# Kernel optimization log

Hardware: AMD Instinct MI355X
Metric: run time of the kernel (lower is better)

The kernel has to match this reference:

```python
import jax, jax.numpy as jnp
import numpy as np

N = 50000      # num_nodes
E = 800000     # num_edges (before self-loops)
IN_C = 128
HID = 64       # per-head channels (concat=False -> heads averaged)
HEADS = 4
OUT_C = 128
NEG_SLOPE = 0.2
EPS = 1e-5


def setup_inputs() -> dict:
    key = jax.random.key(0)
    ks = jax.random.split(key, 12)
    p = lambda k, shape: jax.random.normal(k, shape, dtype=jnp.float32) * 0.1
    inp = {
        "x": jax.random.normal(ks[0], (N, IN_C), dtype=jnp.float32),
        "edge_index": jax.random.randint(ks[1], (2, E), 0, N, dtype=jnp.int32),
        # layer 1 GATConv params
        "W1": p(ks[2], (IN_C, HEADS * HID)),
        "asrc1": p(ks[3], (HEADS, HID)),
        "adst1": p(ks[4], (HEADS, HID)),
        "b1": jnp.zeros((HID,), jnp.float32),
        "g1": jnp.ones((HID,), jnp.float32),
        "be1": jnp.zeros((HID,), jnp.float32),
        # layer 2 GATConv params
        "W2": p(ks[5], (HID, HEADS * HID)),
        "asrc2": p(ks[6], (HEADS, HID)),
        "adst2": p(ks[7], (HEADS, HID)),
        "b2": jnp.zeros((HID,), jnp.float32),
        "g2": jnp.ones((HID,), jnp.float32),
        "be2": jnp.zeros((HID,), jnp.float32),
        # output projection
        "Wo": p(ks[8], (HID, OUT_C)),
        "bo": jnp.zeros((OUT_C,), jnp.float32),
    }
    return inp


def _gat(x, W, asrc, adst, b, src, dst):
    """PyG GATConv (shared lin, concat=False -> mean over heads, + bias)."""
    n = x.shape[0]
    h = (x @ W).reshape(n, HEADS, HID)          # [N,H,C]
    es = jnp.sum(h * asrc, axis=-1)             # [N,H] alpha_src
    ed = jnp.sum(h * adst, axis=-1)             # [N,H] alpha_dst
    e = jax.nn.leaky_relu(es[src] + ed[dst], NEG_SLOPE)  # [E,H]
    # segment softmax over edges grouped by destination node
    emax = jax.ops.segment_max(e, dst, num_segments=n)
    ex = jnp.exp(e - emax[dst])
    den = jax.ops.segment_sum(ex, dst, num_segments=n)
    alpha = ex / den[dst]                       # [E,H]
    msg = h[src] * alpha[:, :, None]            # [E,H,C]
    out = jax.ops.segment_sum(msg, dst, num_segments=n)  # [N,H,C]
    return out.mean(axis=1) + b                 # concat=False -> head mean


def _ln(x, g, b):
    m = x.mean(-1, keepdims=True)
    v = x.var(-1, keepdims=True)
    return (x - m) / jnp.sqrt(v + EPS) * g + b


def reference(x, edge_index, W1, asrc1, adst1, b1, g1, be1,
              W2, asrc2, adst2, b2, g2, be2, Wo, bo):
    n = x.shape[0]
    loop = jnp.arange(n, dtype=edge_index.dtype)   # GATConv add_self_loops=True
    src = jnp.concatenate([edge_index[0], loop])
    dst = jnp.concatenate([edge_index[1], loop])
    h = jax.nn.relu(_ln(_gat(x, W1, asrc1, adst1, b1, src, dst), g1, be1))
    h = jax.nn.relu(_ln(_gat(h, W2, asrc2, adst2, b2, src, dst), g2, be2))
    return h @ Wo + bo
```

## Files before the change

### kernel.cpp

```cpp
#include <hip/hip_runtime.h>

#define NHEADS 4
#define NEG_SLOPE 0.2f
#define EPS_LN 1e-5f
#define BCAP 64
#define POOLCAP 1536
#define BIN_EPB 8192
#define MAX_NS 800

typedef __attribute__((ext_vector_type(8))) short bf16x8;
typedef __attribute__((ext_vector_type(4))) float f32x4;

__global__ __launch_bounds__(256) void k_init_deg(int* __restrict__ deg, int n) {
    int i = blockIdx.x * 256 + threadIdx.x;
    if (i < n) deg[i] = 1;
}

__global__ __launch_bounds__(256) void k_count(const int* __restrict__ dst, int* __restrict__ deg, int e) {
    int i = blockIdx.x * 256 + threadIdx.x;
    if (i < e) atomicAdd(&deg[dst[i]], 1);
}

__global__ __launch_bounds__(256) void k_scan1(const int* __restrict__ deg, int* __restrict__ rs,
                                               int* __restrict__ bsum, int n) {
    __shared__ int tmp[256];
    int tx = threadIdx.x;
    int i = blockIdx.x * 256 + tx;
    int v = (i < n) ? deg[i] : 0;
    tmp[tx] = v;
    __syncthreads();
    for (int off = 1; off < 256; off <<= 1) {
        int t = (tx >= off) ? tmp[tx - off] : 0;
        __syncthreads();
        tmp[tx] += t;
        __syncthreads();
    }
    if (i < n) rs[i] = tmp[tx] - v;
    if (tx == 255) bsum[blockIdx.x] = tmp[255];
}

__global__ __launch_bounds__(256) void k_scan2(int* __restrict__ bsum, int nb) {
    __shared__ int tmp[256];
    int tx = threadIdx.x;
    int v = (tx < nb) ? bsum[tx] : 0;
    tmp[tx] = v;
    __syncthreads();
    for (int off = 1; off < 256; off <<= 1) {
        int t = (tx >= off) ? tmp[tx - off] : 0;
        __syncthreads();
        tmp[tx] += t;
        __syncthreads();
    }
    if (tx < nb) bsum[tx] = tmp[tx] - v;
}

__global__ __launch_bounds__(256) void k_scan3(int* __restrict__ rs, int* __restrict__ cur,
                                               const int* __restrict__ bsum, int n, int total) {
    int i = blockIdx.x * 256 + threadIdx.x;
    if (i < n) {
        int r = rs[i] + bsum[blockIdx.x];
        rs[i] = r;
        cur[i] = r;
    }
    if (i == 0) rs[n] = total;
}

__global__ __launch_bounds__(256) void k_scatter(const int* __restrict__ src, const int* __restrict__ dst,
                                                 int* __restrict__ cur, int* __restrict__ col, int e, int n) {
    int i = blockIdx.x * 256 + threadIdx.x;
    if (i < e + n) {
        int s, d;
        if (i < e) { s = src[i]; d = dst[i]; }
        else       { s = i - e;  d = i - e;  }
        int p = atomicAdd(&cur[d], 1);
        col[p] = s;
    }
}

__device__ __forceinline__ unsigned short cvt_bf16(float x) {
    unsigned u = __float_as_uint(x);
    u += 0x7fffu + ((u >> 16) & 1u);
    return (unsigned short)(u >> 16);
}

__device__ __forceinline__ unsigned pack2_bf16(float a, float b) {
    return (unsigned)cvt_bf16(a) | ((unsigned)cvt_bf16(b) << 16);
}

__global__ __launch_bounds__(256) void k_bin(const int* __restrict__ e_src, const int* __restrict__ e_dst,
                                             int* __restrict__ cursor, unsigned* __restrict__ pool,
                                             int E, int NS) {
    __shared__ unsigned staged[BIN_EPB];
    __shared__ unsigned short st_sl[BIN_EPB];
    __shared__ int scnt[MAX_NS], sprefix[MAX_NS], scur[MAX_NS], gbase[MAX_NS];
    __shared__ int tsum[256];
    int t = threadIdx.x;
    int b0 = blockIdx.x * BIN_EPB;
    for (int s = t; s < NS; s += 256) { scnt[s] = 0; scur[s] = 0; }
    __syncthreads();
    for (int k = 0; k < BIN_EPB / 256; k++) {
        int i = b0 + k * 256 + t;
        if (i < E) atomicAdd(&scnt[e_dst[i] >> 6], 1);
    }
    __syncthreads();
    int per = (NS + 255) / 256;
    int s0 = t * per;
    int acc = 0;
    for (int k = 0; k < per; k++) { int idx = s0 + k; if (idx < NS) acc += scnt[idx]; }
    tsum[t] = acc;
    __syncthreads();
    for (int off = 1; off < 256; off <<= 1) {
        int v = (t >= off) ? tsum[t - off] : 0;
        __syncthreads();
        tsum[t] += v;
        __syncthreads();
    }
    int run = (t == 0) ? 0 : tsum[t - 1];
    for (int k = 0; k < per; k++) {
        int idx = s0 + k;
        if (idx < NS) { sprefix[idx] = run; run += scnt[idx]; }
    }
    for (int s = t; s < NS; s += 256)
        gbase[s] = atomicAdd(&cursor[s], scnt[s]);
    __syncthreads();
    for (int k = 0; k < BIN_EPB / 256; k++) {
        int i = b0 + k * 256 + t;
        if (i < E) {
            int d = e_dst[i];
            int s = e_src[i];
            int sl = d >> 6;
            int p = atomicAdd(&scur[sl], 1);
            int pos = sprefix[sl] + p;
            staged[pos] = (unsigned)s | ((unsigned)(d & 63) << 20);
            st_sl[pos] = (unsigned short)sl;
        }
    }
    __syncthreads();
    int ec = E - b0; if (ec > BIN_EPB) ec = BIN_EPB; if (ec < 0) ec = 0;
    for (int i = t; i < ec; i += 256) {
        unsigned e = staged[i];
        int sl = st_sl[i];
        int off = i - sprefix[sl];
        int gp = gbase[sl] + off;
        if (gp < POOLCAP) pool[(size_t)sl * POOLCAP + gp] = e;
    }
}

template <int K>
__global__ __launch_bounds__(256) void k_gemm_gat(const float* __restrict__ A, const float* __restrict__ B,
                                                  const float* __restrict__ asrc, const float* __restrict__ adst,
                                                  unsigned short* __restrict__ Hb16, float* __restrict__ es,
                                                  float* __restrict__ ed, int M) {
    __shared__ unsigned short Bt[128][136];
    int tid = threadIdx.x;
    int m0 = blockIdx.x * 128;
    int n0 = blockIdx.y * 128;
    {
        int n = tid & 127;
        int kh = tid >> 7;
        int kbeg = kh * (K >> 1);
        int kend = kbeg + (K >> 1);
        const float* bp = B + n0 + n;
#pragma unroll 4
        for (int k = kbeg; k < kend; k += 4) {
            float b0 = bp[(size_t)k * 256];
            float b1 = bp[(size_t)(k + 1) * 256];
            float b2 = bp[(size_t)(k + 2) * 256];
            float b3 = bp[(size_t)(k + 3) * 256];
            uint2 p;
            p.x = pack2_bf16(b0, b1);
            p.y = pack2_bf16(b2, b3);
            *(uint2*)&Bt[n][k] = p;
        }
    }
    __syncthreads();
    int w = tid >> 6, lane = tid & 63;
    int quad = lane >> 4, col16 = lane & 15;
    int mw = m0 + (w >> 1) * 64;
    int ch = w & 1;
    int head = blockIdx.y * 2 + ch;
    f32x4 acc[4][4] = {};
    constexpr int kc = K >> 5;
#pragma unroll 2
    for (int c = 0; c < kc; c++) {
        int kb = c * 32 + quad * 8;
        bf16x8 afr[4], bfr[4];
#pragma unroll
        for (int i = 0; i < 4; i++) {
            int row = mw + i * 16 + col16;
            if (row >= M) row = M - 1;
            const float* ap = &A[(size_t)row * K + kb];
            float4 a0 = *(const float4*)ap;
            float4 a1 = *(const float4*)(ap + 4);
            bf16x8 t;
            t[0] = (short)cvt_bf16(a0.x); t[1] = (short)cvt_bf16(a0.y);
            t[2] = (short)cvt_bf16(a0.z); t[3] = (short)cvt_bf16(a0.w);
            t[4] = (short)cvt_bf16(a1.x); t[5] = (short)cvt_bf16(a1.y);
            t[6] = (short)cvt_bf16(a1.z); t[7] = (short)cvt_bf16(a1.w);
            afr[i] = t;
        }
#pragma unroll
        for (int j = 0; j < 4; j++)
            bfr[j] = *(const bf16x8*)&Bt[ch * 64 + j * 16 + col16][kb];
#pragma unroll
        for (int i = 0; i < 4; i++)
#pragma unroll
            for (int j = 0; j < 4; j++)
                acc[i][j] = __builtin_amdgcn_mfma_f32_16x16x32_bf16(afr[i], bfr[j], acc[i][j], 0, 0, 0);
    }
    float av[4], dv[4];
#pragma unroll
    for (int j = 0; j < 4; j++) {
        av[j] = asrc[head * 64 + j * 16 + col16];
        dv[j] = adst[head * 64 + j * 16 + col16];
    }
#pragma unroll
    for (int i = 0; i < 4; i++) {
#pragma unroll
        for (int r = 0; r < 4; r++) {
            int m = mw + i * 16 + quad * 4 + r;
            float se = acc[i][0][r] * av[0] + acc[i][1][r] * av[1]
                     + acc[i][2][r] * av[2] + acc[i][3][r] * av[3];
            float sd = acc[i][0][r] * dv[0] + acc[i][1][r] * dv[1]
                     + acc[i][2][r] * dv[2] + acc[i][3][r] * dv[3];
            se += __shfl_xor(se, 1, 64); sd += __shfl_xor(sd, 1, 64);
            se += __shfl_xor(se, 2, 64); sd += __shfl_xor(sd, 2, 64);
            se += __shfl_xor(se, 4, 64); sd += __shfl_xor(sd, 4, 64);
            se += __shfl_xor(se, 8, 64); sd += __shfl_xor(sd, 8, 64);
            if (m < M) {
#pragma unroll
                for (int j = 0; j < 4; j++)
                    Hb16[(size_t)m * 256 + head * 64 + j * 16 + col16] = cvt_bf16(acc[i][j][r]);
                if (col16 == 0) { es[m * 4 + head] = se; ed[m * 4 + head] = sd; }
            }
        }
    }
}

__global__ __launch_bounds__(256) void k_gemm(const float* __restrict__ A, const float* __restrict__ B,
                                              const float* __restrict__ bias, float* __restrict__ C,
                                              int M, int Nn, int K) {
    __shared__ unsigned short Al[128][72];
    __shared__ unsigned short Bt[128][72];
    int tid = threadIdx.x;
    int m0 = blockIdx.x * 128;
    {
        int n = tid & 127;
        int kh = tid >> 7;
        int kbeg = kh * (K >> 1);
        int kend = kbeg + (K >> 1);
        const float* bp = B + n;
        for (int k = kbeg; k < kend; k += 4) {
            float b0 = bp[(size_t)k * Nn];
            float b1 = bp[(size_t)(k + 1) * Nn];
            float b2 = bp[(size_t)(k + 2) * Nn];
            float b3 = bp[(size_t)(k + 3) * Nn];
            uint2 p;
            p.x = pack2_bf16(b0, b1);
            p.y = pack2_bf16(b2, b3);
            *(uint2*)&Bt[n][k] = p;
        }
    }
#pragma unroll
    for (int it = 0; it < 8; it++) {
        int idx = it * 256 + tid;
        int row = idx >> 4;
        int kq = (idx & 15) << 2;
        float4 a4 = make_float4(0.f, 0.f, 0.f, 0.f);
        if (m0 + row < M) a4 = *(const float4*)&A[(size_t)(m0 + row) * 64 + kq];
        uint2 p;
        p.x = pack2_bf16(a4.x, a4.y);
        p.y = pack2_bf16(a4.z, a4.w);
        *(uint2*)&Al[row][kq] = p;
    }
    __syncthreads();
    int w = tid >> 6, lane = tid & 63;
    int quad = lane >> 4, col16 = lane & 15;
    int rw = (w >> 1) * 64;
    int ch = w & 1;
    f32x4 acc[4][4] = {};
    int kc = K >> 5;
    for (int c = 0; c < kc; c++) {
        int kb = c * 32 + quad * 8;
        bf16x8 afr[4], bfr[4];
#pragma unroll
        for (int i = 0; i < 4; i++)
            afr[i] = *(const bf16x8*)&Al[rw + i * 16 + col16][kb];
#pragma unroll
        for (int j = 0; j < 4; j++)
            bfr[j] = *(const bf16x8*)&Bt[ch * 64 + j * 16 + col16][kb];
#pragma unroll
        for (int i = 0; i < 4; i++)
#pragma unroll
            for (int j = 0; j < 4; j++)
                acc[i][j] = __builtin_amdgcn_mfma_f32_16x16x32_bf16(afr[i], bfr[j], acc[i][j], 0, 0, 0);
    }
    int mw = m0 + rw;
    float bv[4];
#pragma unroll
    for (int j = 0; j < 4; j++) bv[j] = bias[ch * 64 + j * 16 + col16];
#pragma unroll
    for (int i = 0; i < 4; i++) {
#pragma unroll
        for (int r = 0; r < 4; r++) {
            int m = mw + i * 16 + quad * 4 + r;
            if (m < M) {
#pragma unroll
                for (int j = 0; j < 4; j++)
                    C[(size_t)m * Nn + ch * 64 + j * 16 + col16] = acc[i][j][r] + bv[j];
            }
        }
    }
}

__global__ __launch_bounds__(512) void k_agg_sliced(const unsigned* __restrict__ Hb, const float* __restrict__ es,
                                                    const float* __restrict__ ed, const unsigned* __restrict__ pool,
                                                    const int* __restrict__ cursor, const float* __restrict__ b,
                                                    const float* __restrict__ g, const float* __restrict__ be,
                                                    float* __restrict__ out, int n) {
    __shared__ unsigned ent[POOLCAP];
    __shared__ int lcnt[64], lbase[65], lcur[64];
    int t = threadIdx.x;
    int sl = blockIdx.x;
    if (t < 64) { lcnt[t] = 0; lcur[t] = 0; }
    __syncthreads();
    int ne = cursor[sl]; if (ne > POOLCAP) ne = POOLCAP;
    for (int i = t; i < ne; i += 512)
        atomicAdd(&lcnt[pool[(size_t)sl * POOLCAP + i] >> 20], 1);
    __syncthreads();
    if (t == 0) {
        int run = 0;
        for (int k = 0; k < 64; k++) { lbase[k] = run; run += lcnt[k]; }
        lbase[64] = run;
    }
    __syncthreads();
    for (int i = t; i < ne; i += 512) {
        unsigned e = pool[(size_t)sl * POOLCAP + i];
        int ln = e >> 20;
        int p = atomicAdd(&lcur[ln], 1);
        ent[lbase[ln] + p] = e & 0xFFFFFu;
    }
    __syncthreads();
    int wv = t >> 6, lane = t & 63;
    int head = lane >> 4, cp = lane & 15;
    for (int j = 0; j < 8; j++) {
        int ln = wv * 8 + j;
        int node = sl * 64 + ln;
        if (node >= n) continue;
        float edv = ed[node * 4 + head];
        float eS = es[node * 4 + head] + edv;
        eS = fmaxf(eS, NEG_SLOPE * eS);
        float wS = __expf(eS);
        uint2 uS = *(const uint2*)&Hb[(size_t)node * 128 + lane * 2];
        float acc0 = wS * __uint_as_float(uS.x << 16);
        float acc1 = wS * __uint_as_float(uS.x & 0xffff0000u);
        float acc2 = wS * __uint_as_float(uS.y << 16);
        float acc3 = wS * __uint_as_float(uS.y & 0xffff0000u);
        float den = wS;
        int i0 = lbase[ln], i1 = lbase[ln] + lcnt[ln];
        int i = i0;
        for (; i + 3 < i1; i += 4) {
            int s0 = ent[i], s1 = ent[i + 1], s2 = ent[i + 2], s3 = ent[i + 3];
            float e0 = es[s0 * 4 + head];
            float e1 = es[s1 * 4 + head];
            float e2 = es[s2 * 4 + head];
            float e3 = es[s3 * 4 + head];
            uint2 u0 = *(const uint2*)&Hb[(size_t)s0 * 128 + lane * 2];
            uint2 u1 = *(const uint2*)&Hb[(size_t)s1 * 128 + lane * 2];
            uint2 u2 = *(const uint2*)&Hb[(size_t)s2 * 128 + lane * 2];
            uint2 u3 = *(const uint2*)&Hb[(size_t)s3 * 128 + lane * 2];
            e0 += edv; e1 += edv; e2 += edv; e3 += edv;
            e0 = fmaxf(e0, NEG_SLOPE * e0);
            e1 = fmaxf(e1, NEG_SLOPE * e1);
            e2 = fmaxf(e2, NEG_SLOPE * e2);
            e3 = fmaxf(e3, NEG_SLOPE * e3);
            float w0 = __expf(e0), w1 = __expf(e1), w2 = __expf(e2), w3 = __expf(e3);
            acc0 += w0 * __uint_as_float(u0.x << 16);
            acc1 += w0 * __uint_as_float(u0.x & 0xffff0000u);
            acc2 += w0 * __uint_as_float(u0.y << 16);
            acc3 += w0 * __uint_as_float(u0.y & 0xffff0000u);
            acc0 += w1 * __uint_as_float(u1.x << 16);
            acc1 += w1 * __uint_as_float(u1.x & 0xffff0000u);
            acc2 += w1 * __uint_as_float(u1.y << 16);
            acc3 += w1 * __uint_as_float(u1.y & 0xffff0000u);
            acc0 += w2 * __uint_as_float(u2.x << 16);
            acc1 += w2 * __uint_as_float(u2.x & 0xffff0000u);
            acc2 += w2 * __uint_as_float(u2.y << 16);
            acc3 += w2 * __uint_as_float(u2.y & 0xffff0000u);
            acc0 += w3 * __uint_as_float(u3.x << 16);
            acc1 += w3 * __uint_as_float(u3.x & 0xffff0000u);
            acc2 += w3 * __uint_as_float(u3.y << 16);
            acc3 += w3 * __uint_as_float(u3.y & 0xffff0000u);
            den += w0 + w1 + w2 + w3;
        }
        for (; i < i1; i++) {
            int s0 = ent[i];
            float e0 = es[s0 * 4 + head] + edv;
            uint2 u0 = *(const uint2*)&Hb[(size_t)s0 * 128 + lane * 2];
            e0 = fmaxf(e0, NEG_SLOPE * e0);
            float w0 = __expf(e0);
            acc0 += w0 * __uint_as_float(u0.x << 16);
            acc1 += w0 * __uint_as_float(u0.x & 0xffff0000u);
            acc2 += w0 * __uint_as_float(u0.y << 16);
            acc3 += w0 * __uint_as_float(u0.y & 0xffff0000u);
            den += w0;
        }
        float rd = 1.f / den;
        float r0 = acc0 * rd, r1 = acc1 * rd, r2 = acc2 * rd, r3 = acc3 * rd;
        r0 += __shfl_xor(r0, 16, 64); r1 += __shfl_xor(r1, 16, 64);
        r2 += __shfl_xor(r2, 16, 64); r3 += __shfl_xor(r3, 16, 64);
        r0 += __shfl_xor(r0, 32, 64); r1 += __shfl_xor(r1, 32, 64);
        r2 += __shfl_xor(r2, 32, 64); r3 += __shfl_xor(r3, 32, 64);
        float4 bb = *(const float4*)&b[cp * 4];
        float v0 = 0.25f * r0 + bb.x;
        float v1 = 0.25f * r1 + bb.y;
        float v2 = 0.25f * r2 + bb.z;
        float v3 = 0.25f * r3 + bb.w;
        float s = v0 + v1 + v2 + v3;
        float q = v0 * v0 + v1 * v1 + v2 * v2 + v3 * v3;
        for (int off = 1; off < 16; off <<= 1) {
            s += __shfl_xor(s, off, 64);
            q += __shfl_xor(q, off, 64);
        }
        float mean = s * (1.f / 64.f);
        float var = q * (1.f / 64.f) - mean * mean;
        float rinv = rsqrtf(var + EPS_LN);
        float4 gg = *(const float4*)&g[cp * 4];
        float4 ee = *(const float4*)&be[cp * 4];
        if (head == 0) {
            float4 y;
            y.x = fmaxf((v0 - mean) * rinv * gg.x + ee.x, 0.f);
            y.y = fmaxf((v1 - mean) * rinv * gg.y + ee.y, 0.f);
            y.z = fmaxf((v2 - mean) * rinv * gg.z + ee.z, 0.f);
            y.w = fmaxf((v3 - mean) * rinv * gg.w + ee.w, 0.f);
            *(float4*)&out[(size_t)node * 64 + cp * 4] = y;
        }
    }
}

__global__ __launch_bounds__(256) void k_gat_aggregate(const unsigned* __restrict__ Hb, const float* __restrict__ es,
                                                       const float* __restrict__ ed, const int* __restrict__ rs,
                                                       const int* __restrict__ col,
                                                       const float* __restrict__ b,
                                                       const float* __restrict__ g, const float* __restrict__ be,
                                                       float* __restrict__ out, int n) {
    int node = blockIdx.x * 4 + (threadIdx.x >> 6);
    int lane = threadIdx.x & 63;
    if (node >= n) return;
    int head = lane >> 4;
    int cp = lane & 15;
    float edv = ed[node * 4 + head];
    float acc0 = 0.f, acc1 = 0.f, acc2 = 0.f, acc3 = 0.f, den = 0.f;
    int i0 = rs[node], i1 = rs[node + 1];
    int i = i0;
    for (; i + 3 < i1; i += 4) {
        int s0 = col[i], s1 = col[i + 1], s2 = col[i + 2], s3 = col[i + 3];
        float e0 = es[s0 * 4 + head];
        float e1 = es[s1 * 4 + head];
        float e2 = es[s2 * 4 + head];
        float e3 = es[s3 * 4 + head];
        uint2 u0 = *(const uint2*)&Hb[(size_t)s0 * 128 + lane * 2];
        uint2 u1 = *(const uint2*)&Hb[(size_t)s1 * 128 + lane * 2];
        uint2 u2 = *(const uint2*)&Hb[(size_t)s2 * 128 + lane * 2];
        uint2 u3 = *(const uint2*)&Hb[(size_t)s3 * 128 + lane * 2];
        e0 += edv; e1 += edv; e2 += edv; e3 += edv;
        e0 = fmaxf(e0, NEG_SLOPE * e0);
        e1 = fmaxf(e1, NEG_SLOPE * e1);
        e2 = fmaxf(e2, NEG_SLOPE * e2);
        e3 = fmaxf(e3, NEG_SLOPE * e3);
        float w0 = __expf(e0), w1 = __expf(e1), w2 = __expf(e2), w3 = __expf(e3);
        acc0 += w0 * __uint_as_float(u0.x << 16);
        acc1 += w0 * __uint_as_float(u0.x & 0xffff0000u);
        acc2 += w0 * __uint_as_float(u0.y << 16);
        acc3 += w0 * __uint_as_float(u0.y & 0xffff0000u);
        acc0 += w1 * __uint_as_float(u1.x << 16);
        acc1 += w1 * __uint_as_float(u1.x & 0xffff0000u);
        acc2 += w1 * __uint_as_float(u1.y << 16);
        acc3 += w1 * __uint_as_float(u1.y & 0xffff0000u);
        acc0 += w2 * __uint_as_float(u2.x << 16);
        acc1 += w2 * __uint_as_float(u2.x & 0xffff0000u);
        acc2 += w2 * __uint_as_float(u2.y << 16);
        acc3 += w2 * __uint_as_float(u2.y & 0xffff0000u);
        acc0 += w3 * __uint_as_float(u3.x << 16);
        acc1 += w3 * __uint_as_float(u3.x & 0xffff0000u);
        acc2 += w3 * __uint_as_float(u3.y << 16);
        acc3 += w3 * __uint_as_float(u3.y & 0xffff0000u);
        den += w0 + w1 + w2 + w3;
    }
    for (; i < i1; i++) {
        int s0 = col[i];
        float e0 = es[s0 * 4 + head] + edv;
        uint2 u0 = *(const uint2*)&Hb[(size_t)s0 * 128 + lane * 2];
        e0 = fmaxf(e0, NEG_SLOPE * e0);
        float w0 = __expf(e0);
        acc0 += w0 * __uint_as_float(u0.x << 16);
        acc1 += w0 * __uint_as_float(u0.x & 0xffff0000u);
        acc2 += w0 * __uint_as_float(u0.y << 16);
        acc3 += w0 * __uint_as_float(u0.y & 0xffff0000u);
        den += w0;
    }
    float rd = 1.f / den;
    float r0 = acc0 * rd, r1 = acc1 * rd, r2 = acc2 * rd, r3 = acc3 * rd;
    r0 += __shfl_xor(r0, 16, 64); r1 += __shfl_xor(r1, 16, 64);
    r2 += __shfl_xor(r2, 16, 64); r3 += __shfl_xor(r3, 16, 64);
    r0 += __shfl_xor(r0, 32, 64); r1 += __shfl_xor(r1, 32, 64);
    r2 += __shfl_xor(r2, 32, 64); r3 += __shfl_xor(r3, 32, 64);
    float4 bb = *(const float4*)&b[cp * 4];
    float v0 = 0.25f * r0 + bb.x;
    float v1 = 0.25f * r1 + bb.y;
    float v2 = 0.25f * r2 + bb.z;
    float v3 = 0.25f * r3 + bb.w;
    float s = v0 + v1 + v2 + v3;
    float q = v0 * v0 + v1 * v1 + v2 * v2 + v3 * v3;
    for (int off = 1; off < 16; off <<= 1) {
        s += __shfl_xor(s, off, 64);
        q += __shfl_xor(q, off, 64);
    }
    float mean = s * (1.f / 64.f);
    float var = q * (1.f / 64.f) - mean * mean;
    float rinv = rsqrtf(var + EPS_LN);
    float4 gg = *(const float4*)&g[cp * 4];
    float4 ee = *(const float4*)&be[cp * 4];
    if (head == 0) {
        float4 y;
        y.x = fmaxf((v0 - mean) * rinv * gg.x + ee.x, 0.f);
        y.y = fmaxf((v1 - mean) * rinv * gg.y + ee.y, 0.f);
        y.z = fmaxf((v2 - mean) * rinv * gg.z + ee.z, 0.f);
        y.w = fmaxf((v3 - mean) * rinv * gg.w + ee.w, 0.f);
        *(float4*)&out[(size_t)node * 64 + cp * 4] = y;
    }
}

extern "C" void kernel_launch(void* const* d_in, const int* in_sizes, int n_in,
                              void* d_out, int out_size, void* d_ws, size_t ws_size,
                              hipStream_t stream) {
    const float* x     = (const float*)d_in[0];
    const int*   eidx  = (const int*)d_in[1];
    const float* W1    = (const float*)d_in[2];
    const float* asrc1 = (const float*)d_in[3];
    const float* adst1 = (const float*)d_in[4];
    const float* b1    = (const float*)d_in[5];
    const float* g1    = (const float*)d_in[6];
    const float* be1   = (const float*)d_in[7];
    const float* W2    = (const float*)d_in[8];
    const float* asrc2 = (const float*)d_in[9];
    const float* adst2 = (const float*)d_in[10];
    const float* b2    = (const float*)d_in[11];
    const float* g2    = (const float*)d_in[12];
    const float* be2   = (const float*)d_in[13];
    const float* Wo    = (const float*)d_in[14];
    const float* bo    = (const float*)d_in[15];

    const int N = in_sizes[0] / 128;
    const int E = in_sizes[1] / 2;
    const int* srcp = eidx;
    const int* dstp = eidx + E;

    unsigned* hb   = (unsigned*)d_ws;
    float* h_small = (float*)(hb + (size_t)N * 128);
    float* es      = h_small + (size_t)N * 64;
    float* ed      = es + (size_t)N * 4;
    int* tail      = (int*)(ed + (size_t)N * 4);

    const int nb = (N + 255) / 256;
    const int nwb = (N + 3) / 4;
    const int mt128 = (N + 127) / 128;
    const int NS = (N + 63) >> 6;

    size_t prefix_bytes = (size_t)((char*)tail - (char*)d_ws);
    size_t pool_need = prefix_bytes + (size_t)NS * POOLCAP * 4 + (size_t)NS * 4;

    unsigned* pool = (unsigned*)tail;
    int* cursor = (int*)(pool + (size_t)NS * POOLCAP);

    int* rowstart = nullptr; int* colarr = nullptr;
    bool pooled = (ws_size >= pool_need) && (NS <= MAX_NS);

    if (pooled) {
        hipMemsetAsync(cursor, 0, (size_t)NS * 4, stream);
        k_bin<<<(E + BIN_EPB - 1) / BIN_EPB, 256, 0, stream>>>(srcp, dstp, cursor, pool, E, NS);
    } else {
        int* deg  = tail;
        rowstart  = deg + N;
        int* cur  = rowstart + (N + 1);
        colarr    = cur + N;
        int* bsum = colarr + (size_t)(E + N);
        k_init_deg<<<nb, 256, 0, stream>>>(deg, N);
        k_count<<<(E + 255) / 256, 256, 0, stream>>>(dstp, deg, E);
        k_scan1<<<nb, 256, 0, stream>>>(deg, rowstart, bsum, N);
        k_scan2<<<1, 256, 0, stream>>>(bsum, nb);
        k_scan3<<<nb, 256, 0, stream>>>(rowstart, cur, bsum, N, E + N);
        k_scatter<<<(E + N + 255) / 256, 256, 0, stream>>>(srcp, dstp, cur, colarr, E, N);
    }

    k_gemm_gat<128><<<dim3(mt128, 2), 256, 0, stream>>>(x, W1, asrc1, adst1,
                                                        (unsigned short*)hb, es, ed, N);
    if (pooled)
        k_agg_sliced<<<NS, 512, 0, stream>>>(hb, es, ed, pool, cursor, b1, g1, be1, h_small, N);
    else
        k_gat_aggregate<<<nwb, 256, 0, stream>>>(hb, es, ed, rowstart, colarr, b1, g1, be1, h_small, N);

    k_gemm_gat<64><<<dim3(mt128, 2), 256, 0, stream>>>(h_small, W2, asrc2, adst2,
                                                       (unsigned short*)hb, es, ed, N);
    if (pooled)
        k_agg_sliced<<<NS, 512, 0, stream>>>(hb, es, ed, pool, cursor, b2, g2, be2, h_small, N);
    else
        k_gat_aggregate<<<nwb, 256, 0, stream>>>(hb, es, ed, rowstart, colarr, b2, g2, be2, h_small, N);

    k_gemm<<<mt128, 256, 0, stream>>>(h_small, Wo, bo, (float*)d_out, N, 128, 64);
}
```

Before: 347.1 us.

## Stage A tile in LDS for GEMM and split aggregation across half-wave edge slots

The GEMM now converts each A tile to bf16 once into shared memory, so the four waves no longer each reload and reconvert overlapping rows from global memory. In the sliced aggregation kernel, each wave handles two edges at a time: each half-wave covers one edge and each lane loads 8 bf16 channels with a uint4, then a cross-half shuffle combines the partial sums before the head-mean and layernorm. The serial prefix over local counts is replaced by a wave shuffle scan. The trade-offs are extra shared memory and barriers in the GEMM, and predicated dummy loads on odd edge counts in aggregation.

```diff
diff --git a/kernel.cpp b/kernel.cpp
--- a/kernel.cpp
+++ b/kernel.cpp
@@ -3,7 +3,6 @@
 #define NHEADS 4
 #define NEG_SLOPE 0.2f
 #define EPS_LN 1e-5f
-#define BCAP 64
 #define POOLCAP 1536
 #define BIN_EPB 8192
 #define MAX_NS 800
@@ -86,6 +85,9 @@
 __device__ __forceinline__ unsigned pack2_bf16(float a, float b) {
     return (unsigned)cvt_bf16(a) | ((unsigned)cvt_bf16(b) << 16);
 }
+
+__device__ __forceinline__ float blo(unsigned u) { return __uint_as_float(u << 16); }
+__device__ __forceinline__ float bhi(unsigned u) { return __uint_as_float(u & 0xffff0000u); }
 
 __global__ __launch_bounds__(256) void k_bin(const int* __restrict__ e_src, const int* __restrict__ e_dst,
                                              int* __restrict__ cursor, unsigned* __restrict__ pool,
@@ -152,6 +154,7 @@
                                                   unsigned short* __restrict__ Hb16, float* __restrict__ es,
                                                   float* __restrict__ ed, int M) {
     __shared__ unsigned short Bt[128][136];
+    __shared__ unsigned short Al[128][72];
     int tid = threadIdx.x;
     int m0 = blockIdx.x * 128;
     int n0 = blockIdx.y * 128;
@@ -173,41 +176,48 @@
             *(uint2*)&Bt[n][k] = p;
         }
     }
-    __syncthreads();
     int w = tid >> 6, lane = tid & 63;
     int quad = lane >> 4, col16 = lane & 15;
-    int mw = m0 + (w >> 1) * 64;
+    int rw = (w >> 1) * 64;
     int ch = w & 1;
     int head = blockIdx.y * 2 + ch;
     f32x4 acc[4][4] = {};
-    constexpr int kc = K >> 5;
-#pragma unroll 2
-    for (int c = 0; c < kc; c++) {
-        int kb = c * 32 + quad * 8;
-        bf16x8 afr[4], bfr[4];
-#pragma unroll
-        for (int i = 0; i < 4; i++) {
-            int row = mw + i * 16 + col16;
-            if (row >= M) row = M - 1;
-            const float* ap = &A[(size_t)row * K + kb];
-            float4 a0 = *(const float4*)ap;
-            float4 a1 = *(const float4*)(ap + 4);
-            bf16x8 t;
-            t[0] = (short)cvt_bf16(a0.x); t[1] = (short)cvt_bf16(a0.y);
-            t[2] = (short)cvt_bf16(a0.z); t[3] = (short)cvt_bf16(a0.w);
-            t[4] = (short)cvt_bf16(a1.x); t[5] = (short)cvt_bf16(a1.y);
-            t[6] = (short)cvt_bf16(a1.z); t[7] = (short)cvt_bf16(a1.w);
-            afr[i] = t;
-        }
-#pragma unroll
-        for (int j = 0; j < 4; j++)
-            bfr[j] = *(const bf16x8*)&Bt[ch * 64 + j * 16 + col16][kb];
-#pragma unroll
-        for (int i = 0; i < 4; i++)
+    constexpr int KH = (K > 64) ? 2 : 1;
+    for (int h = 0; h < KH; h++) {
+        __syncthreads();
+#pragma unroll
+        for (int it = 0; it < 8; it++) {
+            int idx = it * 256 + tid;
+            int row = idx >> 4;
+            int kq = (idx & 15) << 2;
+            float4 a4 = make_float4(0.f, 0.f, 0.f, 0.f);
+            int gr = m0 + row;
+            if (gr < M) a4 = *(const float4*)&A[(size_t)gr * K + h * 64 + kq];
+            uint2 p;
+            p.x = pack2_bf16(a4.x, a4.y);
+            p.y = pack2_bf16(a4.z, a4.w);
+            *(uint2*)&Al[row][kq] = p;
+        }
+        __syncthreads();
+#pragma unroll
+        for (int c = 0; c < 2; c++) {
+            int kbl = c * 32 + quad * 8;
+            int kb = h * 64 + kbl;
+            bf16x8 afr[4], bfr[4];
+#pragma unroll
+            for (int i = 0; i < 4; i++)
+                afr[i] = *(const bf16x8*)&Al[rw + i * 16 + col16][kbl];
 #pragma unroll
             for (int j = 0; j < 4; j++)
-                acc[i][j] = __builtin_amdgcn_mfma_f32_16x16x32_bf16(afr[i], bfr[j], acc[i][j], 0, 0, 0);
-    }
+                bfr[j] = *(const bf16x8*)&Bt[ch * 64 + j * 16 + col16][kb];
+#pragma unroll
+            for (int i = 0; i < 4; i++)
+#pragma unroll
+                for (int j = 0; j < 4; j++)
+                    acc[i][j] = __builtin_amdgcn_mfma_f32_16x16x32_bf16(afr[i], bfr[j], acc[i][j], 0, 0, 0);
+        }
+    }
+    int mw = m0 + rw;
     float av[4], dv[4];
 #pragma unroll
     for (int j = 0; j < 4; j++) {
@@ -328,10 +338,15 @@
     for (int i = t; i < ne; i += 512)
         atomicAdd(&lcnt[pool[(size_t)sl * POOLCAP + i] >> 20], 1);
     __syncthreads();
-    if (t == 0) {
-        int run = 0;
-        for (int k = 0; k < 64; k++) { lbase[k] = run; run += lcnt[k]; }
-        lbase[64] = run;
+    if (t < 64) {
+        int v = lcnt[t];
+        int x = v;
+        for (int off = 1; off < 64; off <<= 1) {
+            int y = __shfl_up(x, off, 64);
+            if (t >= off) x += y;
+        }
+        lbase[t] = x - v;
+        if (t == 63) lbase[64] = x;
     }
     __syncthreads();
     for (int i = t; i < ne; i += 512) {
@@ -342,98 +357,96 @@
     }
     __syncthreads();
     int wv = t >> 6, lane = t & 63;
-    int head = lane >> 4, cp = lane & 15;
+    int slot = lane >> 5;
+    int sub = lane & 31;
+    int headL = sub >> 3;
+    int grp = sub & 7;
     for (int j = 0; j < 8; j++) {
         int ln = wv * 8 + j;
         int node = sl * 64 + ln;
         if (node >= n) continue;
-        float edv = ed[node * 4 + head];
-        float eS = es[node * 4 + head] + edv;
-        eS = fmaxf(eS, NEG_SLOPE * eS);
-        float wS = __expf(eS);
-        uint2 uS = *(const uint2*)&Hb[(size_t)node * 128 + lane * 2];
-        float acc0 = wS * __uint_as_float(uS.x << 16);
-        float acc1 = wS * __uint_as_float(uS.x & 0xffff0000u);
-        float acc2 = wS * __uint_as_float(uS.y << 16);
-        float acc3 = wS * __uint_as_float(uS.y & 0xffff0000u);
-        float den = wS;
-        int i0 = lbase[ln], i1 = lbase[ln] + lcnt[ln];
-        int i = i0;
-        for (; i + 3 < i1; i += 4) {
-            int s0 = ent[i], s1 = ent[i + 1], s2 = ent[i + 2], s3 = ent[i + 3];
-            float e0 = es[s0 * 4 + head];
-            float e1 = es[s1 * 4 + head];
-            float e2 = es[s2 * 4 + head];
-            float e3 = es[s3 * 4 + head];
-            uint2 u0 = *(const uint2*)&Hb[(size_t)s0 * 128 + lane * 2];
-            uint2 u1 = *(const uint2*)&Hb[(size_t)s1 * 128 + lane * 2];
-            uint2 u2 = *(const uint2*)&Hb[(size_t)s2 * 128 + lane * 2];
-            uint2 u3 = *(const uint2*)&Hb[(size_t)s3 * 128 + lane * 2];
-            e0 += edv; e1 += edv; e2 += edv; e3 += edv;
+        float edv = ed[node * 4 + headL];
+        float acc0, acc1, acc2, acc3, acc4, acc5, acc6, acc7, den;
+        if (slot == 0) {
+            float eS = es[node * 4 + headL] + edv;
+            eS = fmaxf(eS, NEG_SLOPE * eS);
+            float wS = __expf(eS);
+            const uint4 u = *(const uint4*)&Hb[(size_t)node * 128 + (sub << 2)];
+            acc0 = wS * blo(u.x); acc1 = wS * bhi(u.x);
+            acc2 = wS * blo(u.y); acc3 = wS * bhi(u.y);
+            acc4 = wS * blo(u.z); acc5 = wS * bhi(u.z);
+            acc6 = wS * blo(u.w); acc7 = wS * bhi(u.w);
+            den = wS;
+        } else {
+            acc0 = acc1 = acc2 = acc3 = acc4 = acc5 = acc6 = acc7 = 0.f;
+            den = 0.f;
+        }
+        int cntn = lcnt[ln];
+        int base = lbase[ln];
+        int npairs = (cntn + 1) >> 1;
+#pragma unroll 2
+        for (int p = 0; p < npairs; p++) {
+            int eidx = (p << 1) + slot;
+            bool valid = eidx < cntn;
+            int ridx = base + (valid ? eidx : 0);
+            int s = valid ? (int)ent[ridx] : node;
+            float e0 = es[s * 4 + headL] + edv;
             e0 = fmaxf(e0, NEG_SLOPE * e0);
-            e1 = fmaxf(e1, NEG_SLOPE * e1);
-            e2 = fmaxf(e2, NEG_SLOPE * e2);
-            e3 = fmaxf(e3, NEG_SLOPE * e3);
-            float w0 = __expf(e0), w1 = __expf(e1), w2 = __expf(e2), w3 = __expf(e3);
-            acc0 += w0 * __uint_as_float(u0.x << 16);
-            acc1 += w0 * __uint_as_float(u0.x & 0xffff0000u);
-            acc2 += w0 * __uint_as_float(u0.y << 16);
-            acc3 += w0 * __uint_as_float(u0.y & 0xffff0000u);
-            acc0 += w1 * __uint_as_float(u1.x << 16);
-            acc1 += w1 * __uint_as_float(u1.x & 0xffff0000u);
-            acc2 += w1 * __uint_as_float(u1.y << 16);
-            acc3 += w1 * __uint_as_float(u1.y & 0xffff0000u);
-            acc0 += w2 * __uint_as_float(u2.x << 16);
-            acc1 += w2 * __uint_as_float(u2.x & 0xffff0000u);
-            acc2 += w2 * __uint_as_float(u2.y << 16);
-            acc3 += w2 * __uint_as_float(u2.y & 0xffff0000u);
-            acc0 += w3 * __uint_as_float(u3.x << 16);
-            acc1 += w3 * __uint_as_float(u3.x & 0xffff0000u);
-            acc2 += w3 * __uint_as_float(u3.y << 16);
-            acc3 += w3 * __uint_as_float(u3.y & 0xffff0000u);
-            den += w0 + w1 + w2 + w3;
-        }
-        for (; i < i1; i++) {
-            int s0 = ent[i];
-            float e0 = es[s0 * 4 + head] + edv;
-            uint2 u0 = *(const uint2*)&Hb[(size_t)s0 * 128 + lane * 2];
-            e0 = fmaxf(e0, NEG_SLOPE * e0);
-            float w0 = __expf(e0);
-            acc0 += w0 * __uint_as_float(u0.x << 16);
-            acc1 += w0 * __uint_as_float(u0.x & 0xffff0000u);
-            acc2 += w0 * __uint_as_float(u0.y << 16);
-            acc3 += w0 * __uint_as_float(u0.y & 0xffff0000u);
-            den += w0;
-        }
+            float wgt = valid ? __expf(e0) : 0.f;
+            const uint4 u = *(const uint4*)&Hb[(size_t)s * 128 + (sub << 2)];
+            acc0 += wgt * blo(u.x); acc1 += wgt * bhi(u.x);
+            acc2 += wgt * blo(u.y); acc3 += wgt * bhi(u.y);
+            acc4 += wgt * blo(u.z); acc5 += wgt * bhi(u.z);
+            acc6 += wgt * blo(u.w); acc7 += wgt * bhi(u.w);
+            den += wgt;
+        }
+        acc0 += __shfl_xor(acc0, 32, 64); acc1 += __shfl_xor(acc1, 32, 64);
+        acc2 += __shfl_xor(acc2, 32, 64); acc3 += __shfl_xor(acc3, 32, 64);
+        acc4 += __shfl_xor(acc4, 32, 64); acc5 += __shfl_xor(acc5, 32, 64);
+        acc6 += __shfl_xor(acc6, 32, 64); acc7 += __shfl_xor(acc7, 32, 64);
+        den += __shfl_xor(den, 32, 64);
         float rd = 1.f / den;
-        float r0 = acc0 * rd, r1 = acc1 * rd, r2 = acc2 * rd, r3 = acc3 * rd;
-        r0 += __shfl_xor(r0, 16, 64); r1 += __shfl_xor(r1, 16, 64);
-        r2 += __shfl_xor(r2, 16, 64); r3 += __shfl_xor(r3, 16, 64);
-        r0 += __shfl_xor(r0, 32, 64); r1 += __shfl_xor(r1, 32, 64);
-        r2 += __shfl_xor(r2, 32, 64); r3 += __shfl_xor(r3, 32, 64);
-        float4 bb = *(const float4*)&b[cp * 4];
-        float v0 = 0.25f * r0 + bb.x;
-        float v1 = 0.25f * r1 + bb.y;
-        float v2 = 0.25f * r2 + bb.z;
-        float v3 = 0.25f * r3 + bb.w;
-        float s = v0 + v1 + v2 + v3;
-        float q = v0 * v0 + v1 * v1 + v2 * v2 + v3 * v3;
-        for (int off = 1; off < 16; off <<= 1) {
-            s += __shfl_xor(s, off, 64);
-            q += __shfl_xor(q, off, 64);
-        }
-        float mean = s * (1.f / 64.f);
-        float var = q * (1.f / 64.f) - mean * mean;
+        float v0 = acc0 * rd, v1 = acc1 * rd, v2 = acc2 * rd, v3 = acc3 * rd;
+        float v4 = acc4 * rd, v5 = acc5 * rd, v6 = acc6 * rd, v7 = acc7 * rd;
+        v0 += __shfl_xor(v0, 8, 64);  v1 += __shfl_xor(v1, 8, 64);
+        v2 += __shfl_xor(v2, 8, 64);  v3 += __shfl_xor(v3, 8, 64);
+        v4 += __shfl_xor(v4, 8, 64);  v5 += __shfl_xor(v5, 8, 64);
+        v6 += __shfl_xor(v6, 8, 64);  v7 += __shfl_xor(v7, 8, 64);
+        v0 += __shfl_xor(v0, 16, 64); v1 += __shfl_xor(v1, 16, 64);
+        v2 += __shfl_xor(v2, 16, 64); v3 += __shfl_xor(v3, 16, 64);
+        v4 += __shfl_xor(v4, 16, 64); v5 += __shfl_xor(v5, 16, 64);
+        v6 += __shfl_xor(v6, 16, 64); v7 += __shfl_xor(v7, 16, 64);
+        float4 bbA = *(const float4*)&b[grp * 8];
+        float4 bbB = *(const float4*)&b[grp * 8 + 4];
+        v0 = 0.25f * v0 + bbA.x; v1 = 0.25f * v1 + bbA.y;
+        v2 = 0.25f * v2 + bbA.z; v3 = 0.25f * v3 + bbA.w;
+        v4 = 0.25f * v4 + bbB.x; v5 = 0.25f * v5 + bbB.y;
+        v6 = 0.25f * v6 + bbB.z; v7 = 0.25f * v7 + bbB.w;
+        float s1 = v0 + v1 + v2 + v3 + v4 + v5 + v6 + v7;
+        float s2 = v0 * v0 + v1 * v1 + v2 * v2 + v3 * v3
+                 + v4 * v4 + v5 * v5 + v6 * v6 + v7 * v7;
+        s1 += __shfl_xor(s1, 1, 64); s2 += __shfl_xor(s2, 1, 64);
+        s1 += __shfl_xor(s1, 2, 64); s2 += __shfl_xor(s2, 2, 64);
+        s1 += __shfl_xor(s1, 4, 64); s2 += __shfl_xor(s2, 4, 64);
+        float mean = s1 * (1.f / 64.f);
+        float var = s2 * (1.f / 64.f) - mean * mean;
         float rinv = rsqrtf(var + EPS_LN);
-        float4 gg = *(const float4*)&g[cp * 4];
-        float4 ee = *(const float4*)&be[cp * 4];
-        if (head == 0) {
-            float4 y;
-            y.x = fmaxf((v0 - mean) * rinv * gg.x + ee.x, 0.f);
-            y.y = fmaxf((v1 - mean) * rinv * gg.y + ee.y, 0.f);
-            y.z = fmaxf((v2 - mean) * rinv * gg.z + ee.z, 0.f);
-            y.w = fmaxf((v3 - mean) * rinv * gg.w + ee.w, 0.f);
-            *(float4*)&out[(size_t)node * 64 + cp * 4] = y;
+        if (lane < 8) {
+            float4 ggA = *(const float4*)&g[grp * 8];
+            float4 ggB = *(const float4*)&g[grp * 8 + 4];
+            float4 eeA = *(const float4*)&be[grp * 8];
+            float4 eeB = *(const float4*)&be[grp * 8 + 4];
+            float4 yA, yB;
+            yA.x = fmaxf((v0 - mean) * rinv * ggA.x + eeA.x, 0.f);
+            yA.y = fmaxf((v1 - mean) * rinv * ggA.y + eeA.y, 0.f);
+            yA.z = fmaxf((v2 - mean) * rinv * ggA.z + eeA.z, 0.f);
+            yA.w = fmaxf((v3 - mean) * rinv * ggA.w + eeA.w, 0.f);
+            yB.x = fmaxf((v4 - mean) * rinv * ggB.x + eeB.x, 0.f);
+            yB.y = fmaxf((v5 - mean) * rinv * ggB.y + eeB.y, 0.f);
+            yB.z = fmaxf((v6 - mean) * rinv * ggB.z + eeB.z, 0.f);
+            yB.w = fmaxf((v7 - mean) * rinv * ggB.w + eeB.w, 0.f);
+            *(float4*)&out[(size_t)node * 64 + grp * 8] = yA;
+            *(float4*)&out[(size_t)node * 64 + grp * 8 + 4] = yB;
         }
     }
 }
@@ -469,22 +482,14 @@
         e2 = fmaxf(e2, NEG_SLOPE * e2);
         e3 = fmaxf(e3, NEG_SLOPE * e3);
         float w0 = __expf(e0), w1 = __expf(e1), w2 = __expf(e2), w3 = __expf(e3);
-        acc0 += w0 * __uint_as_float(u0.x << 16);
-        acc1 += w0 * __uint_as_float(u0.x & 0xffff0000u);
-        acc2 += w0 * __uint_as_float(u0.y << 16);
-        acc3 += w0 * __uint_as_float(u0.y & 0xffff0000u);
-        acc0 += w1 * __uint_as_float(u1.x << 16);
-        acc1 += w1 * __uint_as_float(u1.x & 0xffff0000u);
-        acc2 += w1 * __uint_as_float(u1.y << 16);
-        acc3 += w1 * __uint_as_float(u1.y & 0xffff0000u);
-        acc0 += w2 * __uint_as_float(u2.x << 16);
-        acc1 += w2 * __uint_as_float(u2.x & 0xffff0000u);
-        acc2 += w2 * __uint_as_float(u2.y << 16);
-        acc3 += w2 * __uint_as_float(u2.y & 0xffff0000u);
-        acc0 += w3 * __uint_as_float(u3.x << 16);
-        acc1 += w3 * __uint_as_float(u3.x & 0xffff0000u);
-        acc2 += w3 * __uint_as_float(u3.y << 16);
-        acc3 += w3 * __uint_as_float(u3.y & 0xffff0000u);
+        acc0 += w0 * blo(u0.x); acc1 += w0 * bhi(u0.x);
+        acc2 += w0 * blo(u0.y); acc3 += w0 * bhi(u0.y);
+        acc0 += w1 * blo(u1.x); acc1 += w1 * bhi(u1.x);
+        acc2 += w1 * blo(u1.y); acc3 += w1 * bhi(u1.y);
+        acc0 += w2 * blo(u2.x); acc1 += w2 * bhi(u2.x);
+        acc2 += w2 * blo(u2.y); acc3 += w2 * bhi(u2.y);
+        acc0 += w3 * blo(u3.x); acc1 += w3 * bhi(u3.x);
+        acc2 += w3 * blo(u3.y); acc3 += w3 * bhi(u3.y);
         den += w0 + w1 + w2 + w3;
     }
     for (; i < i1; i++) {
@@ -493,10 +498,8 @@
         uint2 u0 = *(const uint2*)&Hb[(size_t)s0 * 128 + lane * 2];
         e0 = fmaxf(e0, NEG_SLOPE * e0);
         float w0 = __expf(e0);
-        acc0 += w0 * __uint_as_float(u0.x << 16);
-        acc1 += w0 * __uint_as_float(u0.x & 0xffff0000u);
-        acc2 += w0 * __uint_as_float(u0.y << 16);
-        acc3 += w0 * __uint_as_float(u0.y & 0xffff0000u);
+        acc0 += w0 * blo(u0.x); acc1 += w0 * bhi(u0.x);
+        acc2 += w0 * blo(u0.y); acc3 += w0 * bhi(u0.y);
         den += w0;
     }
     float rd = 1.f / den;
```

New measurement: 340.3 us. About the same (-2.0%).
